# Kernel optimization log

Measured on AMD Instinct MI355X. Metric: run time of the kernel, lower is better.

The kernel has to match this reference:

```python
import jax, jax.numpy as jnp
import numpy as np

EPS = 1e-20
TAU = 0.1
N_SINK_ITER = 10
N_SAMPLES = 8
SIM_SCALE = 50.0
MISS_MATCH_VALUE = -1.0
N_NODES = 1000
D = 256
N_EDGES = 16000


def setup_inputs() -> dict:
    key = jax.random.key(0)
    ks = jax.random.split(key, 8)
    x_s = jax.random.normal(ks[0], (N_NODES, D), dtype=jnp.float32)
    x_t = jax.random.normal(ks[1], (N_NODES, D), dtype=jnp.float32)
    edge_index_s = jax.random.randint(ks[2], (2, N_EDGES), 0, N_NODES)
    edge_index_t = jax.random.randint(ks[3], (2, N_EDGES), 0, N_NODES)
    scale = 1.0 / np.sqrt(D)
    W1 = jax.random.normal(ks[4], (D, D), dtype=jnp.float32) * scale
    b1 = jnp.zeros((D,), dtype=jnp.float32)
    W2 = jax.random.normal(ks[5], (D, D), dtype=jnp.float32) * scale
    b2 = jnp.zeros((D,), dtype=jnp.float32)
    return {"x_s": x_s, "edge_index_s": edge_index_s, "x_t": x_t,
            "edge_index_t": edge_index_t, "W1": W1, "b1": b1,
            "W2": W2, "b2": b2, "T": 2}


def f_update(x, importance, src, dst, W1, b1, W2, b2):
    # GIN-style update with importance reweighting (reconstructed f_update).
    n = x.shape[0]
    h = x * importance                                   # [n, d]
    agg = jax.ops.segment_sum(h[src], dst, num_segments=n)
    h = jax.nn.relu((h + agg) @ W1 + b1)
    agg = jax.ops.segment_sum(h[src], dst, num_segments=n)
    return (h + agg) @ W2 + b2


def gumbel_sinkhorn(key, log_alpha, tau, n_iter, n_samples):
    # log_alpha: [N, M] -> theta: [n_samples, N, M]
    u = jax.random.uniform(key, (n_samples,) + log_alpha.shape, dtype=log_alpha.dtype)
    gumbel = -jnp.log(-jnp.log(u + EPS) + EPS)
    la = (log_alpha[None, :, :] + gumbel) / tau
    for _ in range(n_iter):
        la = la - jax.nn.logsumexp(la, axis=-1, keepdims=True)
        la = la - jax.nn.logsumexp(la, axis=-2, keepdims=True)
    return jnp.exp(la)


def reward_general(n1, n2, e1, e2, theta, miss_match_value=-1.0):
    # Edge-consistency reward (reconstructed): matched = sum over edge pairs
    # (i,j) in E1, (k,l) in E2 of theta[i,k]*theta[j,l], computed sparsely;
    # unmatched edges in either graph are penalized with miss_match_value.
    th = theta[:, :n1, :n2]                               # [S, n1, n2]
    # W[:, :, k] = sum over target edges (k,l) of th[:, :, l]
    W = jnp.zeros_like(th).at[:, :, e2[0]].add(th[:, :, e2[1]])
    matched = jnp.sum(W[:, e1[0], :] * th[:, e1[1], :], axis=(-1, -2))  # [S]
    num_e1 = e1.shape[1]
    num_e2 = e2.shape[1]
    r = matched + miss_match_value * ((num_e1 - matched) + (num_e2 - matched))
    return jnp.mean(r) / float(num_e1)


def reference(x_s, edge_index_s, x_t, edge_index_t, W1, b1, W2, b2, T):
    n1, n2 = x_s.shape[0], x_t.shape[0]
    src_s, dst_s = edge_index_s[0], edge_index_s[1]
    src_t, dst_t = edge_index_t[0], edge_index_t[1]
    key = jax.random.key(42)

    best_reward = jnp.float32(-jnp.inf)
    loss = jnp.float32(0.0)
    loss_count = jnp.float32(0.0)
    theta_prev = jnp.zeros((n1, n2), dtype=x_s.dtype)
    best_logits = jnp.zeros((n1 + n2, n2 + n1), dtype=x_s.dtype)

    for it in range(T):
        if it == 0:
            imp_s = jnp.ones((n1, 1), dtype=x_s.dtype)
            imp_t = jnp.ones((n2, 1), dtype=x_s.dtype)
        else:
            imp_s = theta_prev.sum(-1, keepdims=True)        # [n1, 1]
            imp_t = theta_prev.sum(-2, keepdims=True).T      # [n2, 1]
        h_s = f_update(x_s, imp_s, src_s, dst_s, W1, b1, W2, b2)
        h_t = f_update(x_t, imp_t, src_t, dst_t, W1, b1, W2, b2)
        h_s = h_s / jnp.linalg.norm(h_s, axis=-1, keepdims=True)
        h_t = h_t / jnp.linalg.norm(h_t, axis=-1, keepdims=True)
        log_alpha = (h_s @ h_t.T) * SIM_SCALE                # [n1, n2]
        log_alpha_ = jnp.pad(log_alpha, ((0, n2), (0, n1)))  # [n1+n2, n2+n1]
        key, sub = jax.random.split(key)
        theta_new = gumbel_sinkhorn(sub, log_alpha_, TAU, N_SINK_ITER, N_SAMPLES)
        r = reward_general(n1, n2, edge_index_s, edge_index_t, theta_new,
                           MISS_MATCH_VALUE)
        improved = r > best_reward
        best_reward = jnp.where(improved, r, best_reward)
        loss = loss - jnp.where(improved, r, jnp.float32(0.0))
        loss_count = loss_count + improved.astype(jnp.float32)
        theta_prev = jnp.where(
            improved,
            jax.lax.stop_gradient(theta_new[:, :n1, :n2].mean(0)),
            theta_prev)
        best_logits = jnp.where(improved, jax.lax.stop_gradient(log_alpha_),
                                best_logits)
    return best_logits, loss / loss_count
```

## Files before the change

### kernel.cpp

```cpp
#include <hip/hip_runtime.h>
#include <stdint.h>
#include <math.h>

#define N_NODES 1000
#define DIM 256
#define N_EDGES 16000
#define NS 8
#define P 2000
#define IC2 100
#define RPC (P / IC2)
#define ICB 200
#define RPB (P / ICB)
#define GR 5

__host__ __device__ inline void tf2x32(uint32_t k0, uint32_t k1,
                                       uint32_t x0, uint32_t x1,
                                       uint32_t* o0, uint32_t* o1) {
  const uint32_t ks2 = k0 ^ k1 ^ 0x1BD11BDAu;
  uint32_t a = x0 + k0, b = x1 + k1;
#define RL(v, d) (((v) << (d)) | ((v) >> (32 - (d))))
#define RND(r) { a += b; b = RL(b, r); b ^= a; }
  RND(13) RND(15) RND(26) RND(6)
  a += k1;  b += ks2 + 1u;
  RND(17) RND(29) RND(16) RND(24)
  a += ks2; b += k0 + 2u;
  RND(13) RND(15) RND(26) RND(6)
  a += k0;  b += k1 + 3u;
  RND(17) RND(29) RND(16) RND(24)
  a += k1;  b += ks2 + 4u;
  RND(13) RND(15) RND(26) RND(6)
  a += ks2; b += k0 + 5u;
#undef RND
#undef RL
  *o0 = a; *o1 = b;
}

__device__ inline float gumbel_from_idx(uint32_t k0, uint32_t k1, uint32_t idx) {
  uint32_t b0, b1;
  tf2x32(k0, k1, 0u, idx, &b0, &b1);
  uint32_t bits = b0 ^ b1;
  float u = __uint_as_float((bits >> 9) | 0x3f800000u) - 1.0f;
  return -__logf(-__logf(u + 1e-20f) + 1e-20f);
}

__device__ inline float blockSum256(float v) {
  __shared__ float sm[4];
  #pragma unroll
  for (int off = 32; off; off >>= 1) v += __shfl_down(v, off, 64);
  if ((threadIdx.x & 63) == 0) sm[threadIdx.x >> 6] = v;
  __syncthreads();
  float r = (sm[0] + sm[1]) + (sm[2] + sm[3]);
  __syncthreads();
  return r;
}
__device__ inline float blockMax256(float v) {
  __shared__ float sm[4];
  #pragma unroll
  for (int off = 32; off; off >>= 1) v = fmaxf(v, __shfl_down(v, off, 64));
  if ((threadIdx.x & 63) == 0) sm[threadIdx.x >> 6] = v;
  __syncthreads();
  float r = fmaxf(fmaxf(sm[0], sm[1]), fmaxf(sm[2], sm[3]));
  __syncthreads();
  return r;
}

__global__ void k_hist(const int* __restrict__ key, int* __restrict__ cnt) {
  int k = blockIdx.x * 256 + threadIdx.x;
  if (k < N_EDGES) atomicAdd(&cnt[key[k]], 1);
}
__global__ void k_scan(const int* __restrict__ cnt, int* __restrict__ start) {
  __shared__ int sm[1024];
  int t = threadIdx.x;
  sm[t] = (t < N_NODES) ? cnt[t] : 0;
  __syncthreads();
  for (int off = 1; off < 1024; off <<= 1) {
    int v = (t >= off) ? sm[t - off] : 0;
    __syncthreads();
    sm[t] += v;
    __syncthreads();
  }
  if (t < N_NODES) start[t + 1] = sm[t];
  if (t == 0) start[0] = 0;
}
__global__ void k_scatter(const int* __restrict__ key, const int* __restrict__ start,
                          int* __restrict__ cursor, int* __restrict__ ids) {
  int k = blockIdx.x * 256 + threadIdx.x;
  if (k < N_EDGES) {
    int c = key[k];
    int slot = start[c] + atomicAdd(&cursor[c], 1);
    ids[slot] = k;
  }
}
__global__ void k_partfill(const int* __restrict__ ids, const int* __restrict__ pv,
                           int* __restrict__ part) {
  int s = blockIdx.x * 256 + threadIdx.x;
  if (s < N_EDGES) part[s] = pv[ids[s]];
}
__global__ void k_packD(const int* __restrict__ startB, const int* __restrict__ partB,
                        int* __restrict__ epackD) {
  int d = blockIdx.x * 256 + threadIdx.x;
  if (d >= N_NODES) return;
  int e0 = startB[d], e1 = startB[d + 1];
  for (int q = e0; q < e1; ++q) epackD[q] = (d << 10) | partB[q];
}

__global__ void k_ones(float* imp) {
  int t = blockIdx.x * 256 + threadIdx.x;
  if (t < 2048) imp[t] = 1.0f;
}

__global__ void k_rowsum(const float* __restrict__ thp, float* __restrict__ imp) {
  int i = blockIdx.x;
  float a = 0.f;
  for (int j = threadIdx.x; j < N_NODES; j += 256) a += thp[(size_t)i * N_NODES + j];
  float s = blockSum256(a);
  if (threadIdx.x == 0) imp[i] = s;
}

__global__ void k_colsum(const float* __restrict__ thp, float* __restrict__ imp) {
  int j = blockIdx.x * 256 + threadIdx.x;
  if (j >= N_NODES) return;
  int r0 = blockIdx.y * 125;
  float a = 0.f;
  for (int i = r0; i < r0 + 125; ++i) a += thp[(size_t)i * N_NODES + j];
  atomicAdd(&imp[1024 + j], a);
}

__global__ void k_scale_b(const float* __restrict__ xs, const float* __restrict__ xt,
                          const float* __restrict__ imp, float* __restrict__ h) {
  int g = blockIdx.y, i = blockIdx.x, d = threadIdx.x;
  const float* x = g ? xt : xs;
  h[(size_t)g * 256000 + i * DIM + d] = x[i * DIM + d] * imp[g * 1024 + i];
}

__global__ void k_agg_b(const float* __restrict__ h, const int* __restrict__ start,
                        const int* __restrict__ part, float* __restrict__ agg) {
  int g = blockIdx.y, i = blockIdx.x, d = threadIdx.x;
  const int* st = start + g * 1008;
  const int* pt = part + g * 16000;
  const float* hh = h + (size_t)g * 256000;
  int e0 = st[i], e1 = st[i + 1];
  float a = 0.f;
  for (int q = e0; q < e1; ++q) a += hh[(size_t)pt[q] * DIM + d];
  agg[(size_t)g * 256000 + i * DIM + d] = a;
}

__global__ void __launch_bounds__(256) k_lin_b(const float* __restrict__ h_,
    const float* __restrict__ agg_, const float* __restrict__ Wm,
    const float* __restrict__ bias, float* __restrict__ out_, int relu) {
  __shared__ float As[16][64];
  __shared__ float Ws[64][64];
  int g = blockIdx.z;
  const float* h   = h_   + (size_t)g * 256000;
  const float* agg = agg_ + (size_t)g * 256000;
  float* out       = out_ + (size_t)g * 256000;
  int tx = threadIdx.x & 63;
  int ty = threadIdx.x >> 6;
  int row0 = blockIdx.x * 16;
  int col0 = blockIdx.y * 64;
  float acc[4] = {0.f, 0.f, 0.f, 0.f};
  for (int kc = 0; kc < DIM; kc += 64) {
    for (int t = threadIdx.x; t < 16 * 64; t += 256) {
      int r = t >> 6, c = t & 63;
      int gr = row0 + r;
      As[r][c] = (gr < N_NODES) ? (h[gr * DIM + kc + c] + agg[gr * DIM + kc + c]) : 0.f;
    }
    for (int t = threadIdx.x; t < 64 * 64; t += 256) {
      int r = t >> 6, c = t & 63;
      Ws[r][c] = Wm[(kc + r) * DIM + col0 + c];
    }
    __syncthreads();
    #pragma unroll 8
    for (int kk = 0; kk < 64; ++kk) {
      float w = Ws[kk][tx];
      acc[0] += As[ty][kk] * w;
      acc[1] += As[ty + 4][kk] * w;
      acc[2] += As[ty + 8][kk] * w;
      acc[3] += As[ty + 12][kk] * w;
    }
    __syncthreads();
  }
  int col = col0 + tx;
  float bv = bias[col];
  #pragma unroll
  for (int r = 0; r < 4; ++r) {
    int gr = row0 + ty + r * 4;
    if (gr < N_NODES) {
      float vv = acc[r] + bv;
      if (relu) vv = fmaxf(vv, 0.f);
      out[gr * DIM + col] = vv;
    }
  }
}

__global__ void k_norm_b(const float* __restrict__ h, float* __restrict__ out) {
  int g = blockIdx.y, i = blockIdx.x;
  float x = h[(size_t)g * 256000 + i * DIM + threadIdx.x];
  float ss = blockSum256(x * x);
  float nrm = sqrtf(ss);
  out[(size_t)g * 256000 + i * DIM + threadIdx.x] = x / nrm;
}

__global__ void __launch_bounds__(256) k_gemm50(const float* __restrict__ A,
    const float* __restrict__ B, float* __restrict__ C) {
  __shared__ float As[64][33];
  __shared__ float Bs[64][33];
  int tr = threadIdx.x >> 4;
  int tc = threadIdx.x & 15;
  int i0 = blockIdx.x * 64, j0 = blockIdx.y * 64;
  float acc[4][4] = {};
  for (int kc = 0; kc < DIM; kc += 32) {
    for (int t = threadIdx.x; t < 64 * 32; t += 256) {
      int r = t >> 5, c = t & 31;
      int gi = i0 + r; As[r][c] = (gi < N_NODES) ? A[gi * DIM + kc + c] : 0.f;
      int gj = j0 + r; Bs[r][c] = (gj < N_NODES) ? B[gj * DIM + kc + c] : 0.f;
    }
    __syncthreads();
    for (int kk = 0; kk < 32; ++kk) {
      float a[4], b[4];
      #pragma unroll
      for (int q = 0; q < 4; ++q) a[q] = As[tr * 4 + q][kk];
      #pragma unroll
      for (int q = 0; q < 4; ++q) b[q] = Bs[tc * 4 + q][kk];
      #pragma unroll
      for (int r = 0; r < 4; ++r)
        #pragma unroll
        for (int c = 0; c < 4; ++c) acc[r][c] += a[r] * b[c];
    }
    __syncthreads();
  }
  for (int r = 0; r < 4; ++r) {
    int gi = i0 + tr * 4 + r;
    if (gi >= N_NODES) continue;
    for (int c = 0; c < 4; ++c) {
      int gj = j0 + tc * 4 + c;
      if (gj < N_NODES) C[(size_t)gi * N_NODES + gj] = 50.0f * acc[r][c];
    }
  }
}

__global__ void __launch_bounds__(256) k_build(const float* __restrict__ la,
    float* __restrict__ base, float* __restrict__ u, float* __restrict__ ps,
    uint32_t k0, uint32_t k1) {
  int ic = blockIdx.x, s = blockIdx.y;
  int t = threadIdx.x;
  int j0 = t * 8;
  bool act = (j0 < P);
  float acc[8] = {0.f,0.f,0.f,0.f,0.f,0.f,0.f,0.f};
  for (int r = 0; r < RPB; ++r) {
    int i = ic * RPB + r;
    float bv[8];
    float lmax = -INFINITY;
    if (act) {
      uint32_t idxbase = (uint32_t)((s * P + i) * P + j0);
      #pragma unroll
      for (int q = 0; q < 8; ++q) {
        int j = j0 + q;
        float g = gumbel_from_idx(k0, k1, idxbase + (uint32_t)q);
        float lav = (i < N_NODES && j < N_NODES) ? la[(size_t)i * N_NODES + j] : 0.0f;
        bv[q] = (lav + g) * 10.0f;
        lmax = fmaxf(lmax, bv[q]);
      }
      float4* p = (float4*)(base + ((size_t)s * P + i) * P + j0);
      p[0] = make_float4(bv[0], bv[1], bv[2], bv[3]);
      p[1] = make_float4(bv[4], bv[5], bv[6], bv[7]);
    }
    float M = blockMax256(lmax);
    float e[8];
    float ls = 0.f;
    if (act) {
      #pragma unroll
      for (int q = 0; q < 8; ++q) { e[q] = __expf(bv[q] - M); ls += e[q]; }
    }
    float S = blockSum256(ls);
    if (t == 0) u[s * P + i] = M + __logf(S);
    if (act) {
      float rs = 1.0f / S;
      #pragma unroll
      for (int q = 0; q < 8; ++q) acc[q] += e[q] * rs;
    }
  }
  if (act) {
    float* pp = ps + ((size_t)(s * ICB + ic)) * 2048 + j0;
    ((float4*)pp)[0] = make_float4(acc[0], acc[1], acc[2], acc[3]);
    ((float4*)pp)[1] = make_float4(acc[4], acc[5], acc[6], acc[7]);
  }
}

__global__ void __launch_bounds__(256) k_fused(const float* __restrict__ base,
    const float* __restrict__ v, float* __restrict__ u, float* __restrict__ ps) {
  int ic = blockIdx.x, s = blockIdx.y;
  int t = threadIdx.x;
  int lane = t & 63, wave = t >> 6;
  int j0 = t * 8;
  bool act = (j0 < P);
  __shared__ float pr[GR][4];
  __shared__ float Sr[GR];
  float vr[8];
  if (act) {
    float4 v0 = *(const float4*)(v + s * P + j0);
    float4 v1 = *(const float4*)(v + s * P + j0 + 4);
    vr[0]=v0.x; vr[1]=v0.y; vr[2]=v0.z; vr[3]=v0.w;
    vr[4]=v1.x; vr[5]=v1.y; vr[6]=v1.z; vr[7]=v1.w;
  }
  float acc[8] = {0.f,0.f,0.f,0.f,0.f,0.f,0.f,0.f};
  for (int g = 0; g < RPC / GR; ++g) {
    float e[GR][8];
    #pragma unroll
    for (int r = 0; r < GR; ++r) {
      int i = ic * RPC + g * GR + r;
      float uo = u[s * P + i];
      float ls = 0.f;
      if (act) {
        const float* brow = base + ((size_t)s * P + i) * P + j0;
        float4 b0 = *(const float4*)brow;
        float4 b1 = *(const float4*)(brow + 4);
        e[r][0] = __expf(b0.x - uo - vr[0]);
        e[r][1] = __expf(b0.y - uo - vr[1]);
        e[r][2] = __expf(b0.z - uo - vr[2]);
        e[r][3] = __expf(b0.w - uo - vr[3]);
        e[r][4] = __expf(b1.x - uo - vr[4]);
        e[r][5] = __expf(b1.y - uo - vr[5]);
        e[r][6] = __expf(b1.z - uo - vr[6]);
        e[r][7] = __expf(b1.w - uo - vr[7]);
        #pragma unroll
        for (int q = 0; q < 8; ++q) ls += e[r][q];
      }
      #pragma unroll
      for (int off = 32; off; off >>= 1) ls += __shfl_down(ls, off, 64);
      if (lane == 0) pr[r][wave] = ls;
    }
    __syncthreads();
    if (t < GR) {
      float S = (pr[t][0] + pr[t][1]) + (pr[t][2] + pr[t][3]);
      Sr[t] = S;
      u[s * P + ic * RPC + g * GR + t] += __logf(S);
    }
    __syncthreads();
    if (act) {
      #pragma unroll
      for (int r = 0; r < GR; ++r) {
        float rs = 1.0f / Sr[r];
        #pragma unroll
        for (int q = 0; q < 8; ++q) acc[q] += e[r][q] * rs;
      }
    }
  }
  if (act) {
    float* pp = ps + ((size_t)(s * IC2 + ic)) * 2048 + j0;
    ((float4*)pp)[0] = make_float4(acc[0], acc[1], acc[2], acc[3]);
    ((float4*)pp)[1] = make_float4(acc[4], acc[5], acc[6], acc[7]);
  }
}

__global__ void k_combine(const float* __restrict__ ps, float* __restrict__ v) {
  int j = blockIdx.x * 256 + threadIdx.x;
  int s = blockIdx.y;
  if (j >= P) return;
  float S = 0.f;
  for (int c = 0; c < IC2; ++c) S += ps[((size_t)(s * IC2 + c)) * 2048 + j];
  v[s * P + j] += __logf(S);
}

__global__ void k_combineB(const float* __restrict__ ps, float* __restrict__ v) {
  int j = blockIdx.x * 256 + threadIdx.x;
  int s = blockIdx.y;
  if (j >= P) return;
  float S = 0.f;
  for (int c = 0; c < ICB; ++c) S += ps[((size_t)(s * ICB + c)) * 2048 + j];
  v[s * P + j] += __logf(S);
}

__global__ void __launch_bounds__(256) k_theta_mean(const float* __restrict__ base,
    const float* __restrict__ u, const float* __restrict__ v,
    float* __restrict__ th, float* __restrict__ thp) {
  int i = blockIdx.x, t = threadIdx.x;
  if (t >= 250) return;
  int j0 = t * 4;
  float4 acc = make_float4(0.f, 0.f, 0.f, 0.f);
  #pragma unroll
  for (int s = 0; s < NS; ++s) {
    float ui = u[s * P + i];
    float4 b = *(const float4*)(base + ((size_t)s * P + i) * P + j0);
    float4 vv = *(const float4*)(v + s * P + j0);
    float4 t4;
    t4.x = __expf(b.x - ui - vv.x);
    t4.y = __expf(b.y - ui - vv.y);
    t4.z = __expf(b.z - ui - vv.z);
    t4.w = __expf(b.w - ui - vv.w);
    *(float4*)(th + ((size_t)s * N_NODES + i) * N_NODES + j0) = t4;
    acc.x += t4.x; acc.y += t4.y; acc.z += t4.z; acc.w += t4.w;
  }
  acc.x *= 0.125f; acc.y *= 0.125f; acc.z *= 0.125f; acc.w *= 0.125f;
  *(float4*)(thp + (size_t)i * N_NODES + j0) = acc;
}

__global__ void __launch_bounds__(256) k_reward(const float* __restrict__ th,
    const int* __restrict__ startA, const int* __restrict__ partA,
    const int* __restrict__ epackD, float* __restrict__ matched) {
  __shared__ float yrow[N_NODES];
  __shared__ float xrow[N_NODES];
  int s = blockIdx.x & 7, b = blockIdx.x >> 3;
  int t = threadIdx.x;
  const float* xr = th + ((size_t)s * N_NODES + b) * N_NODES;
  float4 y4 = make_float4(0.f, 0.f, 0.f, 0.f);
  if (t < 250) {
    ((float4*)xrow)[t] = ((const float4*)xr)[t];
    int e0 = startA[b], e1 = startA[b + 1];
    for (int q = e0; q < e1; ++q) {
      float4 vv = ((const float4*)(th + ((size_t)s * N_NODES + partA[q]) * N_NODES))[t];
      y4.x += vv.x; y4.y += vv.y; y4.z += vv.z; y4.w += vv.w;
    }
    ((float4*)yrow)[t] = y4;
  }
  __syncthreads();
  float acc = 0.f;
  for (int m = t; m < N_EDGES; m += 256) {
    int pk = epackD[m];
    acc += yrow[pk >> 10] * xrow[pk & 1023];
  }
  float ssum = blockSum256(acc);
  if (t == 0) atomicAdd(matched + s, ssum);
}

__global__ void k_fin0(const float* __restrict__ matched, float* __restrict__ scal) {
  if (threadIdx.x == 0) {
    float accm = 0.f;
    for (int s = 0; s < NS; ++s) {
      float m = matched[s];
      float rv = m + (-1.0f) * ((16000.0f - m) + (16000.0f - m));
      accm += rv;
    }
    scal[0] = (accm / 8.0f) / 16000.0f;
  }
}

__global__ void k_fin1(const float* __restrict__ matched, float* __restrict__ scal,
                       float* __restrict__ out) {
  if (threadIdx.x == 0) {
    float accm = 0.f;
    for (int s = 0; s < NS; ++s) {
      float m = matched[s];
      float rv = m + (-1.0f) * ((16000.0f - m) + (16000.0f - m));
      accm += rv;
    }
    float r1 = (accm / 8.0f) / 16000.0f;
    float r0 = scal[0];
    int improved = (r1 > r0) ? 1 : 0;
    scal[1] = r1;
    scal[2] = (float)improved;
    float loss = -r0 - (improved ? r1 : 0.f);
    float cnt = improved ? 2.0f : 1.0f;
    out[(size_t)P * P] = loss / cnt;
  }
}

__global__ void k_out_sel(const float* __restrict__ laA, const float* __restrict__ laB,
                          const float* __restrict__ scal, float* __restrict__ out) {
  int q = blockIdx.x * 256 + threadIdx.x;
  if (q >= P * P / 4) return;
  const float* la = (scal[2] != 0.0f) ? laB : laA;
  int row = q / (P / 4);
  int jc = (q % (P / 4)) * 4;
  float4 vv = make_float4(0.f, 0.f, 0.f, 0.f);
  if (row < N_NODES && jc < N_NODES)
    vv = *(const float4*)(la + (size_t)row * N_NODES + jc);
  *(float4*)(out + (size_t)row * P + jc) = vv;
}

extern "C" void kernel_launch(void* const* d_in, const int* in_sizes, int n_in,
                              void* d_out, int out_size, void* d_ws, size_t ws_size,
                              hipStream_t stream) {
  (void)in_sizes; (void)n_in; (void)out_size; (void)ws_size;
  const float* x_s = (const float*)d_in[0];
  const int*   e_s = (const int*)d_in[1];
  const float* x_t = (const float*)d_in[2];
  const int*   e_t = (const int*)d_in[3];
  const float* W1  = (const float*)d_in[4];
  const float* b1  = (const float*)d_in[5];
  const float* W2  = (const float*)d_in[6];
  const float* b2  = (const float*)d_in[7];
  float* out = (float*)d_out;

  float* ws    = (float*)d_ws;
  float* base  = ws;
  float* theta = base + 32000000;
  float* laA   = theta + 8000000;
  float* laB   = laA + 1000000;
  float* thp   = laB + 1000000;
  float* h0    = thp + 1000000;
  float* agg   = h0 + 512000;
  float* h1    = agg + 512000;
  float* h2    = h1 + 512000;
  float* hn    = h2 + 512000;
  float* uarr  = hn + 512000;
  float* varr  = uarr + 16000;
  float* ps    = varr + 16000;
  float* imp   = ps + 3276800;
  float* matched = imp + 2048;
  float* scal  = matched + 16;
  int* ibase  = (int*)(scal + 16);
  int* cnt    = ibase;
  int* cursor = cnt + 1024;
  int* ids    = cursor + 1024;
  int* startA = ids + 16000;
  int* startB = startA + 1008;
  int* partA  = startB + 1008;
  int* partB  = partA + 16000;
  int* epackD = partB + 16000;

  const int* keys[2]  = { e_s + N_EDGES, e_t + N_EDGES };
  const int* parts[2] = { e_s,           e_t           };
  int* outs_s[2] = { startA, startB };
  int* outs_p[2] = { partA,  partB  };
  for (int r = 0; r < 2; ++r) {
    hipMemsetAsync(cnt, 0, 2048 * sizeof(int), stream);
    k_hist<<<63, 256, 0, stream>>>(keys[r], cnt);
    k_scan<<<1, 1024, 0, stream>>>(cnt, outs_s[r]);
    k_scatter<<<63, 256, 0, stream>>>(keys[r], outs_s[r], cursor, ids);
    k_partfill<<<63, 256, 0, stream>>>(ids, parts[r], outs_p[r]);
  }
  k_packD<<<4, 256, 0, stream>>>(startB, partB, epackD);

  uint32_t k0 = 0u, k1 = 42u;
  uint32_t sub[2][2];
  for (int it = 0; it < 2; ++it) {
    uint32_t nk0, nk1, s0, s1;
    tf2x32(k0, k1, 0u, 0u, &nk0, &nk1);
    tf2x32(k0, k1, 0u, 1u, &s0, &s1);
    sub[it][0] = s0; sub[it][1] = s1;
    k0 = nk0; k1 = nk1;
  }

  for (int it = 0; it < 2; ++it) {
    if (it == 0) {
      k_ones<<<8, 256, 0, stream>>>(imp);
    } else {
      k_rowsum<<<N_NODES, 256, 0, stream>>>(thp, imp);
      hipMemsetAsync(imp + 1024, 0, 1024 * sizeof(float), stream);
      k_colsum<<<dim3(4, 8), 256, 0, stream>>>(thp, imp);
    }
    k_scale_b<<<dim3(N_NODES, 2), 256, 0, stream>>>(x_s, x_t, imp, h0);
    k_agg_b<<<dim3(N_NODES, 2), 256, 0, stream>>>(h0, startA, partA, agg);
    k_lin_b<<<dim3(63, 4, 2), 256, 0, stream>>>(h0, agg, W1, b1, h1, 1);
    k_agg_b<<<dim3(N_NODES, 2), 256, 0, stream>>>(h1, startA, partA, agg);
    k_lin_b<<<dim3(63, 4, 2), 256, 0, stream>>>(h1, agg, W2, b2, h2, 0);
    k_norm_b<<<dim3(N_NODES, 2), 256, 0, stream>>>(h2, hn);
    float* la = it ? laB : laA;
    k_gemm50<<<dim3(16, 16), 256, 0, stream>>>(hn, hn + 256000, la);

    hipMemsetAsync(varr, 0, NS * P * sizeof(float), stream);
    k_build<<<dim3(ICB, NS), 256, 0, stream>>>(la, base, uarr, ps,
                                               sub[it][0], sub[it][1]);
    k_combineB<<<dim3(8, NS), 256, 0, stream>>>(ps, varr);
    for (int k = 0; k < 9; ++k) {
      k_fused<<<dim3(IC2, NS), 256, 0, stream>>>(base, varr, uarr, ps);
      k_combine<<<dim3(8, NS), 256, 0, stream>>>(ps, varr);
    }

    k_theta_mean<<<N_NODES, 256, 0, stream>>>(base, uarr, varr, theta, thp);
    hipMemsetAsync(matched, 0, NS * 4, stream);
    k_reward<<<8000, 256, 0, stream>>>(theta, startA, partA, epackD, matched);
    if (it == 0) k_fin0<<<1, 64, 0, stream>>>(matched, scal);
    else         k_fin1<<<1, 64, 0, stream>>>(matched, scal, out);
  }
  k_out_sel<<<3907, 256, 0, stream>>>(laA, laB, scal, out);
}
```

Before: 1.405 ms.

## Store Sinkhorn matrix in bf16 as row-normalized probabilities with multiplicative updates

The build kernel now stores the row-normalized exponentials (post first row-softmax) as bf16 instead of fp32 log-scores. The fused Sinkhorn iterations apply the dual updates multiplicatively with exp(-du) and exp(-dv), so the per-element exp is dropped. Theta is also stored as bf16 for the reward kernel. This halves the memory traffic over the 8x2000x2000 matrix on every iteration. In exchange, the bf16 rounding of sharply peaked probabilities (tau=0.1) may lose precision and accuracy, and small entries may underflow relative to log-domain storage.

```diff
diff --git a/kernel.cpp b/kernel.cpp
--- a/kernel.cpp
+++ b/kernel.cpp
@@ -12,6 +12,15 @@
 #define ICB 200
 #define RPB (P / ICB)
 #define GR 5
+
+__device__ inline unsigned short f2bf(float f) {
+  uint32_t x = __float_as_uint(f);
+  uint32_t r = (x + 0x7FFFu + ((x >> 16) & 1u)) >> 16;
+  return (unsigned short)r;
+}
+__device__ inline float bf2f(unsigned short u) {
+  return __uint_as_float(((uint32_t)u) << 16);
+}
 
 __host__ __device__ inline void tf2x32(uint32_t k0, uint32_t k1,
                                        uint32_t x0, uint32_t x1,
@@ -240,7 +249,7 @@
 }
 
 __global__ void __launch_bounds__(256) k_build(const float* __restrict__ la,
-    float* __restrict__ base, float* __restrict__ u, float* __restrict__ ps,
+    unsigned short* __restrict__ Q, float* __restrict__ ps,
     uint32_t k0, uint32_t k1) {
   int ic = blockIdx.x, s = blockIdx.y;
   int t = threadIdx.x;
@@ -261,9 +270,6 @@
         bv[q] = (lav + g) * 10.0f;
         lmax = fmaxf(lmax, bv[q]);
       }
-      float4* p = (float4*)(base + ((size_t)s * P + i) * P + j0);
-      p[0] = make_float4(bv[0], bv[1], bv[2], bv[3]);
-      p[1] = make_float4(bv[4], bv[5], bv[6], bv[7]);
     }
     float M = blockMax256(lmax);
     float e[8];
@@ -273,11 +279,18 @@
       for (int q = 0; q < 8; ++q) { e[q] = __expf(bv[q] - M); ls += e[q]; }
     }
     float S = blockSum256(ls);
-    if (t == 0) u[s * P + i] = M + __logf(S);
     if (act) {
       float rs = 1.0f / S;
-      #pragma unroll
-      for (int q = 0; q < 8; ++q) acc[q] += e[q] * rs;
+      unsigned short q8[8];
+      #pragma unroll
+      for (int q = 0; q < 8; ++q) {
+        float val = e[q] * rs;
+        acc[q] += val;
+        q8[q] = f2bf(val);
+      }
+      ushort4* qp = (ushort4*)(Q + ((size_t)s * P + i) * P + j0);
+      qp[0] = make_ushort4(q8[0], q8[1], q8[2], q8[3]);
+      qp[1] = make_ushort4(q8[4], q8[5], q8[6], q8[7]);
     }
   }
   if (act) {
@@ -287,8 +300,8 @@
   }
 }
 
-__global__ void __launch_bounds__(256) k_fused(const float* __restrict__ base,
-    const float* __restrict__ v, float* __restrict__ u, float* __restrict__ ps) {
+__global__ void __launch_bounds__(256) k_fused(const unsigned short* __restrict__ Q,
+    const float* __restrict__ dv, float* __restrict__ du, float* __restrict__ ps) {
   int ic = blockIdx.x, s = blockIdx.y;
   int t = threadIdx.x;
   int lane = t & 63, wave = t >> 6;
@@ -296,12 +309,14 @@
   bool act = (j0 < P);
   __shared__ float pr[GR][4];
   __shared__ float Sr[GR];
-  float vr[8];
+  float ev[8];
   if (act) {
-    float4 v0 = *(const float4*)(v + s * P + j0);
-    float4 v1 = *(const float4*)(v + s * P + j0 + 4);
-    vr[0]=v0.x; vr[1]=v0.y; vr[2]=v0.z; vr[3]=v0.w;
-    vr[4]=v1.x; vr[5]=v1.y; vr[6]=v1.z; vr[7]=v1.w;
+    float4 v0 = *(const float4*)(dv + s * P + j0);
+    float4 v1 = *(const float4*)(dv + s * P + j0 + 4);
+    ev[0] = __expf(-v0.x); ev[1] = __expf(-v0.y);
+    ev[2] = __expf(-v0.z); ev[3] = __expf(-v0.w);
+    ev[4] = __expf(-v1.x); ev[5] = __expf(-v1.y);
+    ev[6] = __expf(-v1.z); ev[7] = __expf(-v1.w);
   }
   float acc[8] = {0.f,0.f,0.f,0.f,0.f,0.f,0.f,0.f};
   for (int g = 0; g < RPC / GR; ++g) {
@@ -309,20 +324,20 @@
     #pragma unroll
     for (int r = 0; r < GR; ++r) {
       int i = ic * RPC + g * GR + r;
-      float uo = u[s * P + i];
+      float edu = __expf(-du[s * P + i]);
       float ls = 0.f;
       if (act) {
-        const float* brow = base + ((size_t)s * P + i) * P + j0;
-        float4 b0 = *(const float4*)brow;
-        float4 b1 = *(const float4*)(brow + 4);
-        e[r][0] = __expf(b0.x - uo - vr[0]);
-        e[r][1] = __expf(b0.y - uo - vr[1]);
-        e[r][2] = __expf(b0.z - uo - vr[2]);
-        e[r][3] = __expf(b0.w - uo - vr[3]);
-        e[r][4] = __expf(b1.x - uo - vr[4]);
-        e[r][5] = __expf(b1.y - uo - vr[5]);
-        e[r][6] = __expf(b1.z - uo - vr[6]);
-        e[r][7] = __expf(b1.w - uo - vr[7]);
+        const unsigned short* qrow = Q + ((size_t)s * P + i) * P + j0;
+        ushort4 a = *(const ushort4*)qrow;
+        ushort4 b = *(const ushort4*)(qrow + 4);
+        e[r][0] = bf2f(a.x) * edu * ev[0];
+        e[r][1] = bf2f(a.y) * edu * ev[1];
+        e[r][2] = bf2f(a.z) * edu * ev[2];
+        e[r][3] = bf2f(a.w) * edu * ev[3];
+        e[r][4] = bf2f(b.x) * edu * ev[4];
+        e[r][5] = bf2f(b.y) * edu * ev[5];
+        e[r][6] = bf2f(b.z) * edu * ev[6];
+        e[r][7] = bf2f(b.w) * edu * ev[7];
         #pragma unroll
         for (int q = 0; q < 8; ++q) ls += e[r][q];
       }
@@ -334,7 +349,7 @@
     if (t < GR) {
       float S = (pr[t][0] + pr[t][1]) + (pr[t][2] + pr[t][3]);
       Sr[t] = S;
-      u[s * P + ic * RPC + g * GR + t] += __logf(S);
+      du[s * P + ic * RPC + g * GR + t] += __logf(S);
     }
     __syncthreads();
     if (act) {
@@ -371,45 +386,46 @@
   v[s * P + j] += __logf(S);
 }
 
-__global__ void __launch_bounds__(256) k_theta_mean(const float* __restrict__ base,
-    const float* __restrict__ u, const float* __restrict__ v,
-    float* __restrict__ th, float* __restrict__ thp) {
+__global__ void __launch_bounds__(256) k_theta_mean(const unsigned short* __restrict__ Q,
+    const float* __restrict__ du, const float* __restrict__ dv,
+    unsigned short* __restrict__ th, float* __restrict__ thp) {
   int i = blockIdx.x, t = threadIdx.x;
   if (t >= 250) return;
   int j0 = t * 4;
   float4 acc = make_float4(0.f, 0.f, 0.f, 0.f);
   #pragma unroll
   for (int s = 0; s < NS; ++s) {
-    float ui = u[s * P + i];
-    float4 b = *(const float4*)(base + ((size_t)s * P + i) * P + j0);
-    float4 vv = *(const float4*)(v + s * P + j0);
-    float4 t4;
-    t4.x = __expf(b.x - ui - vv.x);
-    t4.y = __expf(b.y - ui - vv.y);
-    t4.z = __expf(b.z - ui - vv.z);
-    t4.w = __expf(b.w - ui - vv.w);
-    *(float4*)(th + ((size_t)s * N_NODES + i) * N_NODES + j0) = t4;
-    acc.x += t4.x; acc.y += t4.y; acc.z += t4.z; acc.w += t4.w;
+    float duo = du[s * P + i];
+    ushort4 q4 = *(const ushort4*)(Q + ((size_t)s * P + i) * P + j0);
+    float4 vv = *(const float4*)(dv + s * P + j0);
+    float t0 = bf2f(q4.x) * __expf(-duo - vv.x);
+    float t1 = bf2f(q4.y) * __expf(-duo - vv.y);
+    float t2 = bf2f(q4.z) * __expf(-duo - vv.z);
+    float t3 = bf2f(q4.w) * __expf(-duo - vv.w);
+    *(ushort4*)(th + ((size_t)s * N_NODES + i) * N_NODES + j0) =
+        make_ushort4(f2bf(t0), f2bf(t1), f2bf(t2), f2bf(t3));
+    acc.x += t0; acc.y += t1; acc.z += t2; acc.w += t3;
   }
   acc.x *= 0.125f; acc.y *= 0.125f; acc.z *= 0.125f; acc.w *= 0.125f;
   *(float4*)(thp + (size_t)i * N_NODES + j0) = acc;
 }
 
-__global__ void __launch_bounds__(256) k_reward(const float* __restrict__ th,
+__global__ void __launch_bounds__(256) k_reward(const unsigned short* __restrict__ th,
     const int* __restrict__ startA, const int* __restrict__ partA,
     const int* __restrict__ epackD, float* __restrict__ matched) {
   __shared__ float yrow[N_NODES];
   __shared__ float xrow[N_NODES];
   int s = blockIdx.x & 7, b = blockIdx.x >> 3;
   int t = threadIdx.x;
-  const float* xr = th + ((size_t)s * N_NODES + b) * N_NODES;
+  const unsigned short* xr = th + ((size_t)s * N_NODES + b) * N_NODES;
   float4 y4 = make_float4(0.f, 0.f, 0.f, 0.f);
   if (t < 250) {
-    ((float4*)xrow)[t] = ((const float4*)xr)[t];
+    ushort4 x4 = ((const ushort4*)xr)[t];
+    ((float4*)xrow)[t] = make_float4(bf2f(x4.x), bf2f(x4.y), bf2f(x4.z), bf2f(x4.w));
     int e0 = startA[b], e1 = startA[b + 1];
     for (int q = e0; q < e1; ++q) {
-      float4 vv = ((const float4*)(th + ((size_t)s * N_NODES + partA[q]) * N_NODES))[t];
-      y4.x += vv.x; y4.y += vv.y; y4.z += vv.z; y4.w += vv.w;
+      ushort4 v4 = ((const ushort4*)(th + ((size_t)s * N_NODES + partA[q]) * N_NODES))[t];
+      y4.x += bf2f(v4.x); y4.y += bf2f(v4.y); y4.z += bf2f(v4.z); y4.w += bf2f(v4.w);
     }
     ((float4*)yrow)[t] = y4;
   }
@@ -482,10 +498,9 @@
   const float* b2  = (const float*)d_in[7];
   float* out = (float*)d_out;
 
-  float* ws    = (float*)d_ws;
-  float* base  = ws;
-  float* theta = base + 32000000;
-  float* laA   = theta + 8000000;
+  unsigned short* Qbuf  = (unsigned short*)d_ws;
+  unsigned short* theta = Qbuf + 32000000;
+  float* laA   = (float*)(theta + 8000000);
   float* laB   = laA + 1000000;
   float* thp   = laB + 1000000;
   float* h0    = thp + 1000000;
@@ -499,8 +514,7 @@
   float* imp   = ps + 3276800;
   float* matched = imp + 2048;
   float* scal  = matched + 16;
-  int* ibase  = (int*)(scal + 16);
-  int* cnt    = ibase;
+  int* cnt    = (int*)(scal + 16);
   int* cursor = cnt + 1024;
   int* ids    = cursor + 1024;
   int* startA = ids + 16000;
@@ -549,16 +563,16 @@
     float* la = it ? laB : laA;
     k_gemm50<<<dim3(16, 16), 256, 0, stream>>>(hn, hn + 256000, la);
 
-    hipMemsetAsync(varr, 0, NS * P * sizeof(float), stream);
-    k_build<<<dim3(ICB, NS), 256, 0, stream>>>(la, base, uarr, ps,
+    hipMemsetAsync(uarr, 0, 2 * NS * P * sizeof(float), stream);
+    k_build<<<dim3(ICB, NS), 256, 0, stream>>>(la, Qbuf, ps,
                                                sub[it][0], sub[it][1]);
     k_combineB<<<dim3(8, NS), 256, 0, stream>>>(ps, varr);
     for (int k = 0; k < 9; ++k) {
-      k_fused<<<dim3(IC2, NS), 256, 0, stream>>>(base, varr, uarr, ps);
+      k_fused<<<dim3(IC2, NS), 256, 0, stream>>>(Qbuf, varr, uarr, ps);
       k_combine<<<dim3(8, NS), 256, 0, stream>>>(ps, varr);
     }
 
-    k_theta_mean<<<N_NODES, 256, 0, stream>>>(base, uarr, varr, theta, thp);
+    k_theta_mean<<<N_NODES, 256, 0, stream>>>(Qbuf, uarr, varr, theta, thp);
     hipMemsetAsync(matched, 0, NS * 4, stream);
     k_reward<<<8000, 256, 0, stream>>>(theta, startA, partA, epackD, matched);
     if (it == 0) k_fin0<<<1, 64, 0, stream>>>(matched, scal);
```

Result: faster. 1.285 ms (-8.5%).
